# Optimization experiments

Hardware: AMD Instinct MI355X
Metric: run time of the kernel (lower is better)

Reference implementation:

```python
import jax, jax.numpy as jnp
import numpy as np

INPUT_DIM, LATENT_DIM, HIDDEN_DIM, BATCH = 1024, 128, 1024, 32768


def setup_inputs() -> dict:
    key = jax.random.key(0)
    ks = jax.random.split(key, 12)
    s = 0.02
    x = (jax.random.uniform(ks[0], (BATCH, INPUT_DIM)) < 0.5).astype(jnp.float32)  # binary data
    eps = jax.random.normal(ks[1], (BATCH, LATENT_DIM), dtype=jnp.float32)
    return {
        "x": x,
        "eps": eps,
        "We1": jax.random.normal(ks[2], (INPUT_DIM, HIDDEN_DIM)) * s,
        "be1": jnp.zeros((HIDDEN_DIM,), jnp.float32),
        "Wmu": jax.random.normal(ks[3], (HIDDEN_DIM, LATENT_DIM)) * s,
        "bmu": jnp.zeros((LATENT_DIM,), jnp.float32),
        "Wls": jax.random.normal(ks[4], (HIDDEN_DIM, LATENT_DIM)) * s,
        "bls": jnp.zeros((LATENT_DIM,), jnp.float32),
        "Wd1": jax.random.normal(ks[5], (LATENT_DIM, HIDDEN_DIM)) * s,
        "bd1": jnp.zeros((HIDDEN_DIM,), jnp.float32),
        "Wd2": jax.random.normal(ks[6], (HIDDEN_DIM, INPUT_DIM)) * s,
        "bd2": jnp.zeros((INPUT_DIM,), jnp.float32),
    }


def reference(x, eps, We1, be1, Wmu, bmu, Wls, bls, Wd1, bd1, Wd2, bd2):
    # Encoder: one hidden ReLU layer, mu / logsigma heads
    h = jax.nn.relu(x @ We1 + be1)                      # [B, H]
    mu = h @ Wmu + bmu                                  # [B, L]
    logsigma = h @ Wls + bls                            # [B, L]
    # Reparameterization: z = sigma * eps + mu (vectorized diag(exp(logsigma)) @ eps)
    z = mu + jnp.exp(logsigma) * eps                    # [B, L]
    # Decoder: one hidden ReLU layer, sigmoid Bernoulli params
    hd = jax.nn.relu(z @ Wd1 + bd1)                     # [B, H]
    theta = jax.nn.sigmoid(hd @ Wd2 + bd2)              # [B, D]
    # Bernoulli log-likelihood: sum_j log(theta^x * (1-theta)^(1-x))
    log_px = jnp.sum(x * jnp.log(theta) + (1.0 - x) * jnp.log1p(-theta), axis=-1)  # [B]
    # KL(q||N(0,I)) = 0.5 * sum(sigma^2 + mu^2 - log(sigma^2) - 1)
    kl = 0.5 * jnp.sum(jnp.exp(2.0 * logsigma) + mu * mu - 2.0 * logsigma - 1.0, axis=-1)  # [B]
    return log_px - kl                                  # elbo_mc [B]
```

## Files before the change

kernel.cpp:

```cpp
#include <hip/hip_runtime.h>
#include <cstdint>
#include <cstddef>


typedef __bf16 bf16x8 __attribute__((ext_vector_type(8)));
typedef float f32x4 __attribute__((ext_vector_type(4)));

__device__ __forceinline__ unsigned short f32_to_bf16(float f) {
  unsigned int u = __float_as_uint(f);
  u += 0x7fffu + ((u >> 16) & 1u);
  return (unsigned short)(u >> 16);
}

__global__ void cast_bf16_k(const float* __restrict__ in,
                            unsigned short* __restrict__ out, int n4) {
  int stride = gridDim.x * blockDim.x;
  for (int i = blockIdx.x * blockDim.x + threadIdx.x; i < n4; i += stride) {
    float4 v = reinterpret_cast<const float4*>(in)[i];
    ushort4 o = make_ushort4(f32_to_bf16(v.x), f32_to_bf16(v.y),
                             f32_to_bf16(v.z), f32_to_bf16(v.w));
    reinterpret_cast<ushort4*>(out)[i] = o;
  }
}

struct TransJob { const float* in; unsigned short* out; int K, N, blkEnd; };

__global__ void transpose_all_k(TransJob j0, TransJob j1, TransJob j2,
                                TransJob j3, TransJob j4) {
  __shared__ float tile[32][33];
  int bid = blockIdx.x;
  TransJob j; int base;
  if (bid < j0.blkEnd)      { j = j0; base = 0; }
  else if (bid < j1.blkEnd) { j = j1; base = j0.blkEnd; }
  else if (bid < j2.blkEnd) { j = j2; base = j1.blkEnd; }
  else if (bid < j3.blkEnd) { j = j3; base = j2.blkEnd; }
  else                      { j = j4; base = j3.blkEnd; }
  int local = bid - base;
  int gxN = j.N >> 5;
  int n0 = (local % gxN) * 32, k0 = (local / gxN) * 32;
  int tx = threadIdx.x, ty = threadIdx.y;
#pragma unroll
  for (int r = 0; r < 32; r += 8)
    tile[ty + r][tx] = j.in[(size_t)(k0 + ty + r) * j.N + n0 + tx];
  __syncthreads();
#pragma unroll
  for (int r = 0; r < 32; r += 8)
    j.out[(size_t)(n0 + ty + r) * j.K + k0 + tx] = f32_to_bf16(tile[tx][ty + r]);
}

__device__ __forceinline__ void gl_lds16(const unsigned short* g, unsigned short* l) {
  __builtin_amdgcn_global_load_lds(
      (__attribute__((address_space(1))) void*)g,
      (__attribute__((address_space(3))) void*)l, 16, 0, 0);
}

template <int EPI>
__global__ __launch_bounds__(256) void gemm_bt(
    const unsigned short* __restrict__ A, const unsigned short* __restrict__ BT,
    int gx, int N, int K,
    const float* __restrict__ bias0, const float* __restrict__ bias1,
    unsigned short* __restrict__ outb, float* __restrict__ outf,
    const unsigned short* __restrict__ xbf) {
  __shared__ __align__(16) unsigned short As[128 * 32];
  __shared__ __align__(16) unsigned short Bs[128 * 32];

  const int tid = threadIdx.x;
  const int lane = tid & 63;
  const int wave = tid >> 6;
  const int wr = wave >> 1, wc = wave & 1;
  const int bid = blockIdx.x;
  const int xcd = bid & 7;
  const int t8 = bid >> 3;
  const int m0 = (xcd + 8 * (t8 / gx)) * 128;
  const int n0 = (t8 % gx) * 128;
  const int lm = lane & 15, lq = lane >> 4;

  const int c0 = tid;
  const int row0 = c0 >> 2, q0 = (c0 & 3) ^ ((row0 >> 1) & 3);
  const int c1 = 256 + tid;
  const int row1 = c1 >> 2, q1 = (c1 & 3) ^ ((row1 >> 1) & 3);
  const unsigned short* agp0 = A + (size_t)(m0 + row0) * K + q0 * 8;
  const unsigned short* agp1 = A + (size_t)(m0 + row1) * K + q1 * 8;
  const unsigned short* bgp0 = BT + (size_t)(n0 + row0) * K + q0 * 8;
  const unsigned short* bgp1 = BT + (size_t)(n0 + row1) * K + q1 * 8;

  const int aslot = (lq ^ ((lm >> 1) & 3)) * 8;

  f32x4 acc[4][4] = {};

  for (int kt = 0; kt < K; kt += 32) {
    gl_lds16(agp0 + kt, As + c0 * 8);
    gl_lds16(agp1 + kt, As + c1 * 8);
    gl_lds16(bgp0 + kt, Bs + c0 * 8);
    gl_lds16(bgp1 + kt, Bs + c1 * 8);
    __syncthreads();

    bf16x8 af[4], bfr[4];
#pragma unroll
    for (int i = 0; i < 4; ++i)
      af[i] = *reinterpret_cast<const bf16x8*>(As + (wr * 64 + i * 16 + lm) * 32 + aslot);
#pragma unroll
    for (int j = 0; j < 4; ++j)
      bfr[j] = *reinterpret_cast<const bf16x8*>(Bs + (wc * 64 + j * 16 + lm) * 32 + aslot);
#pragma unroll
    for (int i = 0; i < 4; ++i)
#pragma unroll
      for (int j = 0; j < 4; ++j)
        acc[i][j] = __builtin_amdgcn_mfma_f32_16x16x32_bf16(af[i], bfr[j], acc[i][j], 0, 0, 0);
    __syncthreads();
  }

  if (EPI == 0) {
#pragma unroll
    for (int i = 0; i < 4; ++i)
#pragma unroll
      for (int j = 0; j < 4; ++j) {
        int col = n0 + wc * 64 + j * 16 + lm;
        float bias = bias0[col];
#pragma unroll
        for (int r = 0; r < 4; ++r) {
          int row = m0 + wr * 64 + i * 16 + lq * 4 + r;
          float v = acc[i][j][r] + bias;
          v = fmaxf(v, 0.f);
          outb[(size_t)row * N + col] = f32_to_bf16(v);
        }
      }
  } else if (EPI == 1) {
#pragma unroll
    for (int i = 0; i < 4; ++i)
#pragma unroll
      for (int j = 0; j < 4; ++j) {
        int col = n0 + wc * 64 + j * 16 + lm;
        float bias = (col < 128) ? bias0[col] : bias1[col - 128];
#pragma unroll
        for (int r = 0; r < 4; ++r) {
          int row = m0 + wr * 64 + i * 16 + lq * 4 + r;
          outf[(size_t)row * N + col] = acc[i][j][r] + bias;
        }
      }
  } else {
#pragma unroll
    for (int i = 0; i < 4; ++i) {
      float rs[4] = {0.f, 0.f, 0.f, 0.f};
#pragma unroll
      for (int j = 0; j < 4; ++j) {
        int col = n0 + wc * 64 + j * 16 + lm;
        float bias = bias0[col];
#pragma unroll
        for (int r = 0; r < 4; ++r) {
          int row = m0 + wr * 64 + i * 16 + lq * 4 + r;
          float l = acc[i][j][r] + bias;
          unsigned short xb = xbf[(size_t)row * N + col];
          float t = xb ? -l : l;
          float sp = fmaxf(t, 0.f) + __logf(1.f + __expf(-fabsf(t)));
          rs[r] -= sp;
        }
      }
#pragma unroll
      for (int off = 1; off < 16; off <<= 1)
#pragma unroll
        for (int r = 0; r < 4; ++r) rs[r] += __shfl_xor(rs[r], off, 64);
      if (lm == 0) {
#pragma unroll
        for (int r = 0; r < 4; ++r)
          atomicAdd(&outf[m0 + wr * 64 + i * 16 + lq * 4 + r], rs[r]);
      }
    }
  }
}

__global__ __launch_bounds__(256) void zkl_k(const float* __restrict__ S2,
                                             const float* __restrict__ eps,
                                             unsigned short* __restrict__ z,
                                             float* __restrict__ out) {
  int wave = threadIdx.x >> 6, lane = threadIdx.x & 63;
  int b = blockIdx.x * 4 + wave;
  float2 mu = reinterpret_cast<const float2*>(S2 + (size_t)b * 256)[lane];
  float2 ls = reinterpret_cast<const float2*>(S2 + (size_t)b * 256 + 128)[lane];
  float2 ep = reinterpret_cast<const float2*>(eps + (size_t)b * 128)[lane];
  float z0 = fmaf(__expf(ls.x), ep.x, mu.x);
  float z1 = fmaf(__expf(ls.y), ep.y, mu.y);
  reinterpret_cast<ushort2*>(z + (size_t)b * 128)[lane] =
      make_ushort2(f32_to_bf16(z0), f32_to_bf16(z1));
  float kt = 0.5f * (__expf(2.f * ls.x) + mu.x * mu.x - 2.f * ls.x - 1.f) +
             0.5f * (__expf(2.f * ls.y) + mu.y * mu.y - 2.f * ls.y - 1.f);
#pragma unroll
  for (int off = 32; off > 0; off >>= 1) kt += __shfl_down(kt, off, 64);
  if (lane == 0) out[b] = -kt;
}

extern "C" void kernel_launch(void* const* d_in, const int* in_sizes, int n_in,
                              void* d_out, int out_size, void* d_ws, size_t ws_size,
                              hipStream_t stream) {
  const float* x   = (const float*)d_in[0];
  const float* eps = (const float*)d_in[1];
  const float* We1 = (const float*)d_in[2];
  const float* be1 = (const float*)d_in[3];
  const float* Wmu = (const float*)d_in[4];
  const float* bmu = (const float*)d_in[5];
  const float* Wls = (const float*)d_in[6];
  const float* bls = (const float*)d_in[7];
  const float* Wd1 = (const float*)d_in[8];
  const float* bd1 = (const float*)d_in[9];
  const float* Wd2 = (const float*)d_in[10];
  const float* bd2 = (const float*)d_in[11];
  float* out = (float*)d_out;

  const int B = 32768, D = 1024, H = 1024, L = 128;

  char* ws = (char*)d_ws;
  size_t off = 0;
  auto alloc = [&](size_t bytes) {
    void* p = ws + off;
    off += (bytes + 255) & ~(size_t)255;
    return p;
  };
  unsigned short* xbf  = (unsigned short*)alloc((size_t)B * D * 2);
  unsigned short* w1t  = (unsigned short*)alloc((size_t)H * D * 2);
  unsigned short* w2t  = (unsigned short*)alloc((size_t)256 * H * 2);
  unsigned short* wd1t = (unsigned short*)alloc((size_t)H * L * 2);
  unsigned short* wd2t = (unsigned short*)alloc((size_t)D * H * 2);
  unsigned short* h    = (unsigned short*)alloc((size_t)B * H * 2);
  float*          S2   = (float*)alloc((size_t)B * 256 * 4);
  unsigned short* z    = (unsigned short*)alloc((size_t)B * L * 2);
  unsigned short* hd   = h;

  cast_bf16_k<<<2048, 256, 0, stream>>>(x, xbf, B * D / 4);

  TransJob j0{We1, w1t, D, H, 1024};
  TransJob j1{Wmu, w2t, H, L, 1152};
  TransJob j2{Wls, w2t + 128 * H, H, L, 1280};
  TransJob j3{Wd1, wd1t, L, H, 1408};
  TransJob j4{Wd2, wd2t, H, D, 2432};
  transpose_all_k<<<2432, dim3(32, 8), 0, stream>>>(j0, j1, j2, j3, j4);

  gemm_bt<0><<<8 * 256, 256, 0, stream>>>(
      xbf, w1t, 8, H, D, be1, nullptr, h, nullptr, nullptr);
  gemm_bt<1><<<2 * 256, 256, 0, stream>>>(
      h, w2t, 2, 256, H, bmu, bls, nullptr, S2, nullptr);
  zkl_k<<<B / 4, 256, 0, stream>>>(S2, eps, z, out);
  gemm_bt<0><<<8 * 256, 256, 0, stream>>>(
      z, wd1t, 8, H, L, bd1, nullptr, hd, nullptr, nullptr);
  gemm_bt<2><<<8 * 256, 256, 0, stream>>>(
      hd, wd2t, 8, D, H, bd2, nullptr, nullptr, out, xbf);

  (void)in_sizes; (void)n_in; (void)out_size; (void)ws_size;
}
```

Baseline: 483.0 us.

## Fuse mu/logsigma GEMM with reparameterization and KL, deepen K tile to 64

The mu/logsigma GEMM now runs in a dedicated kernel where each block covers all 256 output columns for 128 rows. Its epilogue computes z and the KL term directly, which removes the fp32 S2 round trip and the separate zkl kernel. The generic GEMM K-step grows from 32 to 64 with an 8-way XOR swizzle, so it needs half as many barriers per K. The trade-off is twice the LDS per block for the generic GEMM, and a heavy-register, occupancy-1 fused kernel launched with only 256 blocks.

```diff
diff --git a/kernel.cpp b/kernel.cpp
--- a/kernel.cpp
+++ b/kernel.cpp
@@ -58,11 +58,11 @@
 __global__ __launch_bounds__(256) void gemm_bt(
     const unsigned short* __restrict__ A, const unsigned short* __restrict__ BT,
     int gx, int N, int K,
-    const float* __restrict__ bias0, const float* __restrict__ bias1,
+    const float* __restrict__ bias0,
     unsigned short* __restrict__ outb, float* __restrict__ outf,
     const unsigned short* __restrict__ xbf) {
-  __shared__ __align__(16) unsigned short As[128 * 32];
-  __shared__ __align__(16) unsigned short Bs[128 * 32];
+  __shared__ __align__(16) unsigned short As[128 * 64];
+  __shared__ __align__(16) unsigned short Bs[128 * 64];
 
   const int tid = threadIdx.x;
   const int lane = tid & 63;
@@ -75,38 +75,43 @@
   const int n0 = (t8 % gx) * 128;
   const int lm = lane & 15, lq = lane >> 4;
 
-  const int c0 = tid;
-  const int row0 = c0 >> 2, q0 = (c0 & 3) ^ ((row0 >> 1) & 3);
-  const int c1 = 256 + tid;
-  const int row1 = c1 >> 2, q1 = (c1 & 3) ^ ((row1 >> 1) & 3);
-  const unsigned short* agp0 = A + (size_t)(m0 + row0) * K + q0 * 8;
-  const unsigned short* agp1 = A + (size_t)(m0 + row1) * K + q1 * 8;
-  const unsigned short* bgp0 = BT + (size_t)(n0 + row0) * K + q0 * 8;
-  const unsigned short* bgp1 = BT + (size_t)(n0 + row1) * K + q1 * 8;
-
-  const int aslot = (lq ^ ((lm >> 1) & 3)) * 8;
+  const unsigned short* agp[4];
+  const unsigned short* bgp[4];
+#pragma unroll
+  for (int r = 0; r < 4; ++r) {
+    int c = tid + 256 * r;
+    int row = c >> 3, q = (c & 7) ^ (row & 7);
+    agp[r] = A + (size_t)(m0 + row) * K + q * 8;
+    bgp[r] = BT + (size_t)(n0 + row) * K + q * 8;
+  }
+  const int sw = lm & 7;
 
   f32x4 acc[4][4] = {};
 
-  for (int kt = 0; kt < K; kt += 32) {
-    gl_lds16(agp0 + kt, As + c0 * 8);
-    gl_lds16(agp1 + kt, As + c1 * 8);
-    gl_lds16(bgp0 + kt, Bs + c0 * 8);
-    gl_lds16(bgp1 + kt, Bs + c1 * 8);
+  for (int kt = 0; kt < K; kt += 64) {
+#pragma unroll
+    for (int r = 0; r < 4; ++r) {
+      gl_lds16(agp[r] + kt, As + (tid + 256 * r) * 8);
+      gl_lds16(bgp[r] + kt, Bs + (tid + 256 * r) * 8);
+    }
     __syncthreads();
 
-    bf16x8 af[4], bfr[4];
-#pragma unroll
-    for (int i = 0; i < 4; ++i)
-      af[i] = *reinterpret_cast<const bf16x8*>(As + (wr * 64 + i * 16 + lm) * 32 + aslot);
-#pragma unroll
-    for (int j = 0; j < 4; ++j)
-      bfr[j] = *reinterpret_cast<const bf16x8*>(Bs + (wc * 64 + j * 16 + lm) * 32 + aslot);
-#pragma unroll
-    for (int i = 0; i < 4; ++i)
+#pragma unroll
+    for (int s = 0; s < 2; ++s) {
+      const int so = ((s << 2) | lq) ^ sw;
+      bf16x8 af[4], bfr[4];
+#pragma unroll
+      for (int i = 0; i < 4; ++i)
+        af[i] = *reinterpret_cast<const bf16x8*>(As + (wr * 64 + i * 16 + lm) * 64 + so * 8);
 #pragma unroll
       for (int j = 0; j < 4; ++j)
-        acc[i][j] = __builtin_amdgcn_mfma_f32_16x16x32_bf16(af[i], bfr[j], acc[i][j], 0, 0, 0);
+        bfr[j] = *reinterpret_cast<const bf16x8*>(Bs + (wc * 64 + j * 16 + lm) * 64 + so * 8);
+#pragma unroll
+      for (int i = 0; i < 4; ++i)
+#pragma unroll
+        for (int j = 0; j < 4; ++j)
+          acc[i][j] = __builtin_amdgcn_mfma_f32_16x16x32_bf16(af[i], bfr[j], acc[i][j], 0, 0, 0);
+    }
     __syncthreads();
   }
 
@@ -123,19 +128,6 @@
           float v = acc[i][j][r] + bias;
           v = fmaxf(v, 0.f);
           outb[(size_t)row * N + col] = f32_to_bf16(v);
-        }
-      }
-  } else if (EPI == 1) {
-#pragma unroll
-    for (int i = 0; i < 4; ++i)
-#pragma unroll
-      for (int j = 0; j < 4; ++j) {
-        int col = n0 + wc * 64 + j * 16 + lm;
-        float bias = (col < 128) ? bias0[col] : bias1[col - 128];
-#pragma unroll
-        for (int r = 0; r < 4; ++r) {
-          int row = m0 + wr * 64 + i * 16 + lq * 4 + r;
-          outf[(size_t)row * N + col] = acc[i][j][r] + bias;
         }
       }
   } else {
@@ -169,24 +161,92 @@
   }
 }
 
-__global__ __launch_bounds__(256) void zkl_k(const float* __restrict__ S2,
-                                             const float* __restrict__ eps,
-                                             unsigned short* __restrict__ z,
-                                             float* __restrict__ out) {
-  int wave = threadIdx.x >> 6, lane = threadIdx.x & 63;
-  int b = blockIdx.x * 4 + wave;
-  float2 mu = reinterpret_cast<const float2*>(S2 + (size_t)b * 256)[lane];
-  float2 ls = reinterpret_cast<const float2*>(S2 + (size_t)b * 256 + 128)[lane];
-  float2 ep = reinterpret_cast<const float2*>(eps + (size_t)b * 128)[lane];
-  float z0 = fmaf(__expf(ls.x), ep.x, mu.x);
-  float z1 = fmaf(__expf(ls.y), ep.y, mu.y);
-  reinterpret_cast<ushort2*>(z + (size_t)b * 128)[lane] =
-      make_ushort2(f32_to_bf16(z0), f32_to_bf16(z1));
-  float kt = 0.5f * (__expf(2.f * ls.x) + mu.x * mu.x - 2.f * ls.x - 1.f) +
-             0.5f * (__expf(2.f * ls.y) + mu.y * mu.y - 2.f * ls.y - 1.f);
-#pragma unroll
-  for (int off = 32; off > 0; off >>= 1) kt += __shfl_down(kt, off, 64);
-  if (lane == 0) out[b] = -kt;
+__global__ __launch_bounds__(256, 1) void gemm2_zkl(
+    const unsigned short* __restrict__ A,
+    const unsigned short* __restrict__ BT,
+    int K,
+    const float* __restrict__ bmu, const float* __restrict__ bls,
+    const float* __restrict__ eps,
+    unsigned short* __restrict__ z,
+    float* __restrict__ out) {
+  __shared__ __align__(16) unsigned short As[128 * 64];
+  __shared__ __align__(16) unsigned short Bs[256 * 64];
+
+  const int tid = threadIdx.x;
+  const int lane = tid & 63;
+  const int wave = tid >> 6;
+  const int m0 = blockIdx.x * 128;
+  const int lm = lane & 15, lq = lane >> 4;
+
+  const unsigned short* agp[4];
+  const unsigned short* bgp[8];
+#pragma unroll
+  for (int r = 0; r < 4; ++r) {
+    int c = tid + 256 * r;
+    int row = c >> 3, q = (c & 7) ^ (row & 7);
+    agp[r] = A + (size_t)(m0 + row) * K + q * 8;
+  }
+#pragma unroll
+  for (int r = 0; r < 8; ++r) {
+    int c = tid + 256 * r;
+    int row = c >> 3, q = (c & 7) ^ (row & 7);
+    bgp[r] = BT + (size_t)row * K + q * 8;
+  }
+  const int sw = lm & 7;
+
+  f32x4 acc[2][16] = {};
+
+  for (int kt = 0; kt < K; kt += 64) {
+#pragma unroll
+    for (int r = 0; r < 4; ++r) gl_lds16(agp[r] + kt, As + (tid + 256 * r) * 8);
+#pragma unroll
+    for (int r = 0; r < 8; ++r) gl_lds16(bgp[r] + kt, Bs + (tid + 256 * r) * 8);
+    __syncthreads();
+
+#pragma unroll
+    for (int s = 0; s < 2; ++s) {
+      const int so = ((s << 2) | lq) ^ sw;
+      bf16x8 af[2];
+#pragma unroll
+      for (int i = 0; i < 2; ++i)
+        af[i] = *reinterpret_cast<const bf16x8*>(As + (wave * 32 + i * 16 + lm) * 64 + so * 8);
+#pragma unroll
+      for (int j = 0; j < 16; ++j) {
+        bf16x8 b = *reinterpret_cast<const bf16x8*>(Bs + (j * 16 + lm) * 64 + so * 8);
+        acc[0][j] = __builtin_amdgcn_mfma_f32_16x16x32_bf16(af[0], b, acc[0][j], 0, 0, 0);
+        acc[1][j] = __builtin_amdgcn_mfma_f32_16x16x32_bf16(af[1], b, acc[1][j], 0, 0, 0);
+      }
+    }
+    __syncthreads();
+  }
+
+#pragma unroll
+  for (int i = 0; i < 2; ++i) {
+    float kl[4] = {0.f, 0.f, 0.f, 0.f};
+#pragma unroll
+    for (int j = 0; j < 8; ++j) {
+      int dim = j * 16 + lm;
+      float bm = bmu[dim], bl = bls[dim];
+#pragma unroll
+      for (int r = 0; r < 4; ++r) {
+        int row = m0 + wave * 32 + i * 16 + lq * 4 + r;
+        float mu = acc[i][j][r] + bm;
+        float ls = acc[i][j + 8][r] + bl;
+        float e = eps[(size_t)row * 128 + dim];
+        z[(size_t)row * 128 + dim] = f32_to_bf16(fmaf(__expf(ls), e, mu));
+        kl[r] += 0.5f * (__expf(2.f * ls) + mu * mu - 2.f * ls - 1.f);
+      }
+    }
+#pragma unroll
+    for (int off = 1; off < 16; off <<= 1)
+#pragma unroll
+      for (int r = 0; r < 4; ++r) kl[r] += __shfl_xor(kl[r], off, 64);
+    if (lm == 0) {
+#pragma unroll
+      for (int r = 0; r < 4; ++r)
+        out[m0 + wave * 32 + i * 16 + lq * 4 + r] = -kl[r];
+    }
+  }
 }
 
 extern "C" void kernel_launch(void* const* d_in, const int* in_sizes, int n_in,
@@ -221,7 +281,6 @@
   unsigned short* wd1t = (unsigned short*)alloc((size_t)H * L * 2);
   unsigned short* wd2t = (unsigned short*)alloc((size_t)D * H * 2);
   unsigned short* h    = (unsigned short*)alloc((size_t)B * H * 2);
-  float*          S2   = (float*)alloc((size_t)B * 256 * 4);
   unsigned short* z    = (unsigned short*)alloc((size_t)B * L * 2);
   unsigned short* hd   = h;
 
@@ -235,14 +294,12 @@
   transpose_all_k<<<2432, dim3(32, 8), 0, stream>>>(j0, j1, j2, j3, j4);
 
   gemm_bt<0><<<8 * 256, 256, 0, stream>>>(
-      xbf, w1t, 8, H, D, be1, nullptr, h, nullptr, nullptr);
-  gemm_bt<1><<<2 * 256, 256, 0, stream>>>(
-      h, w2t, 2, 256, H, bmu, bls, nullptr, S2, nullptr);
-  zkl_k<<<B / 4, 256, 0, stream>>>(S2, eps, z, out);
+      xbf, w1t, 8, H, D, be1, h, nullptr, nullptr);
+  gemm2_zkl<<<B / 128, 256, 0, stream>>>(h, w2t, H, bmu, bls, eps, z, out);
   gemm_bt<0><<<8 * 256, 256, 0, stream>>>(
-      z, wd1t, 8, H, L, bd1, nullptr, hd, nullptr, nullptr);
+      z, wd1t, 8, H, L, bd1, hd, nullptr, nullptr);
   gemm_bt<2><<<8 * 256, 256, 0, stream>>>(
-      hd, wd2t, 8, D, H, bd2, nullptr, nullptr, out, xbf);
+      hd, wd2t, 8, D, H, bd2, nullptr, out, xbf);
 
   (void)in_sizes; (void)n_in; (void)out_size; (void)ws_size;
 }
```

After: 469.1 us. 2.9% less time.
